# Optimization experiments

Measured on AMD Instinct MI355X. Metric: run time of the kernel, lower is better.

The kernel has to match this reference:

```python
import jax, jax.numpy as jnp
import numpy as np


def setup_inputs() -> dict:
    key = jax.random.key(0)
    k1, k2, k3, k4 = jax.random.split(key, 4)
    b, c, h, w = 16, 1024, 32, 32
    dim = h * w  # 1024
    x = jax.random.normal(k1, (b, c, h, w), dtype=jnp.float32)
    cond_img = jax.random.normal(k2, (b, c, h, w), dtype=jnp.float32)
    # torch nn.Linear weights: (out_features, in_features), y = x @ W.T
    Wq = jax.random.normal(k3, (dim, dim), dtype=jnp.float32) * (dim ** -0.5)
    Wkv = jax.random.normal(k4, (2 * dim, dim), dtype=jnp.float32) * (dim ** -0.5)
    return {"x": x, "cond_img": cond_img, "Wq": Wq, "Wkv": Wkv}


def reference(x, cond_img, Wq, Wkv):
    b, c, h, w = x.shape
    dim = h * w
    scale = dim ** -0.5
    xf = x.reshape(b, c, dim)          # (b, c, dim)
    cf = cond_img.reshape(b, c, dim)   # (b, c, dim)
    q = jnp.einsum('bcd,od->bco', xf, Wq)          # (b, c, dim)
    kv = jnp.einsum('bcd,od->bco', cf, Wkv)        # (b, c, 2*dim)
    k, v = jnp.split(kv, 2, axis=-1)               # each (b, c, dim)
    attn = jnp.einsum('bic,bjc->bij', q, k) * scale  # (b, c, c)
    attn = jax.nn.softmax(attn, axis=-1)
    out = jnp.einsum('bij,bjc->bic', attn, v)      # (b, c, dim)
    return out.reshape(b, c, h, w)
```

## Files before the change

### kernel.cpp

```cpp
#include <hip/hip_runtime.h>
#include <stdint.h>


typedef __bf16 bf16_t;
typedef bf16_t bf16x8 __attribute__((ext_vector_type(8)));
typedef float f32x4 __attribute__((ext_vector_type(4)));

#define AS1 __attribute__((address_space(1)))
#define AS3 __attribute__((address_space(3)))

__device__ __forceinline__ uint16_t f2bf(float f) {
  bf16_t h = (bf16_t)f;
  return __builtin_bit_cast(uint16_t, h);
}

__global__ __launch_bounds__(256) void cvt_all(
    const float* __restrict__ x, const float* __restrict__ c,
    const float* __restrict__ wq, const float* __restrict__ wkv,
    uint16_t* __restrict__ XB, uint16_t* __restrict__ CB,
    uint16_t* __restrict__ WQB, uint16_t* __restrict__ WKVB) {
  long i = (long)blockIdx.x * 256 + threadIdx.x;
  if (i >= 9175040) return;
  const float* src;
  uint16_t* dst;
  long off;
  if (i < 4194304) { src = x; dst = XB; off = i; }
  else if (i < 8388608) { src = c; dst = CB; off = i - 4194304; }
  else if (i < 8650752) { src = wq; dst = WQB; off = i - 8388608; }
  else { src = wkv; dst = WKVB; off = i - 8650752; }
  float4 v = ((const float4*)src)[off];
  ushort4 o;
  o.x = f2bf(v.x); o.y = f2bf(v.y); o.z = f2bf(v.z); o.w = f2bf(v.w);
  ((ushort4*)dst)[off] = o;
}

__device__ __forceinline__ void stage_tile(const uint16_t* __restrict__ g,
                                           int ldK, uint16_t* lds, int tid) {
#pragma unroll
  for (int i = 0; i < 4; ++i) {
    int cix = i * 512 + tid;
    int row = cix >> 3;
    int ch = cix & 7;
    int sch = ch ^ (row & 7);
    const uint16_t* gp = g + row * ldK + sch * 8;
    __builtin_amdgcn_global_load_lds((AS1 void*)gp,
                                     (AS3 void*)((uint8_t*)lds + cix * 16), 16,
                                     0, 0);
  }
}

__device__ __forceinline__ void stage128(const uint16_t* __restrict__ g,
                                         int ldK, uint16_t* lds, int tid) {
#pragma unroll
  for (int i = 0; i < 4; ++i) {
    int cix = i * 256 + tid;
    int row = cix >> 3;
    int ch = cix & 7;
    int sch = ch ^ (row & 7);
    const uint16_t* gp = g + row * ldK + sch * 8;
    __builtin_amdgcn_global_load_lds((AS1 void*)gp,
                                     (AS3 void*)((uint8_t*)lds + cix * 16), 16,
                                     0, 0);
  }
}

__device__ __forceinline__ void xcd_decode(int& bx, int& by, int& bz) {
  const int gx = gridDim.x, gy = gridDim.y;
  const int nwg = gx * gy * gridDim.z;
  int fid = blockIdx.x + gx * (blockIdx.y + gy * blockIdx.z);
  int swz = (fid & 7) * (nwg >> 3) + (fid >> 3);
  bx = swz % gx;
  int rem = swz / gx;
  by = rem % gy;
  bz = rem / gy;
}

__global__ __launch_bounds__(512, 2) void g_kv(
    const uint16_t* __restrict__ A, const uint16_t* __restrict__ B,
    uint16_t* __restrict__ Kp, uint16_t* __restrict__ Vp, int K) {
  __shared__ uint16_t smem[65536];

  const int tid = threadIdx.x;
  const int lane = tid & 63;
  const int wid = tid >> 6;
  const int wr = wid >> 2;
  const int wc = wid & 3;
  const int lr = lane & 15, lg = lane >> 4;
  const int ch0 = lr & 7;

  int bx, by, bz;
  xcd_decode(bx, by, bz);
  const int row0 = by * 256;
  const int col0 = bx * 256;
  const uint16_t* At = A + (long long)row0 * K;
  const uint16_t* Bt = B + (long long)col0 * K;

  const int NT = K >> 6;

  stage_tile(At, K, smem, tid);
  stage_tile(Bt, K, smem + 32768, tid);
  stage_tile(At + 64, K, smem + 16384, tid);
  stage_tile(Bt + 64, K, smem + 49152, tid);
  asm volatile("s_waitcnt vmcnt(8)" ::: "memory");
  __builtin_amdgcn_s_barrier();

  f32x4 acc[8][4] = {};
  bf16x8 aA_[4][2], aB_[4][2], bF[4][2];

  {
    const uint8_t* sa = (const uint8_t*)smem;
#pragma unroll
    for (int mi = 0; mi < 4; ++mi)
#pragma unroll
      for (int kk = 0; kk < 2; ++kk)
        aA_[mi][kk] = *(const bf16x8*)(sa + (wr * 128 + mi * 16 + lr) * 128 +
                                       (((kk * 4 + lg) ^ ch0) << 4));
  }

  for (int t = 0; t < NT; ++t) {
    const uint8_t* sa = (const uint8_t*)(smem + (t & 1) * 16384);
    const uint8_t* sb = (const uint8_t*)(smem + 32768 + (t & 1) * 16384);

#pragma unroll
    for (int nj = 0; nj < 4; ++nj)
#pragma unroll
      for (int kk = 0; kk < 2; ++kk)
        bF[nj][kk] = *(const bf16x8*)(sb + (wc * 64 + nj * 16 + lr) * 128 +
                                      (((kk * 4 + lg) ^ ch0) << 4));
#pragma unroll
    for (int mi = 0; mi < 4; ++mi)
#pragma unroll
      for (int kk = 0; kk < 2; ++kk)
        aB_[mi][kk] = *(const bf16x8*)(sa + (wr * 128 + 64 + mi * 16 + lr) * 128 +
                                       (((kk * 4 + lg) ^ ch0) << 4));
    __builtin_amdgcn_s_setprio(1);
#pragma unroll
    for (int kk = 0; kk < 2; ++kk)
#pragma unroll
      for (int mi = 0; mi < 4; ++mi)
#pragma unroll
        for (int nj = 0; nj < 4; ++nj)
          acc[mi][nj] = __builtin_amdgcn_mfma_f32_16x16x32_bf16(
              aA_[mi][kk], bF[nj][kk], acc[mi][nj], 0, 0, 0);
    __builtin_amdgcn_s_setprio(0);
    if (t + 1 < NT) asm volatile("s_waitcnt vmcnt(4)" ::: "memory");
    asm volatile("s_waitcnt lgkmcnt(0)" ::: "memory");
    __builtin_amdgcn_s_barrier();

    if (t + 2 < NT) {
      stage_tile(At + (t + 2) * 64, K, smem + (t & 1) * 16384, tid);
      stage_tile(Bt + (t + 2) * 64, K, smem + 32768 + (t & 1) * 16384, tid);
    }
    if (t + 1 < NT) {
      const uint8_t* sa2 = (const uint8_t*)(smem + ((t + 1) & 1) * 16384);
#pragma unroll
      for (int mi = 0; mi < 4; ++mi)
#pragma unroll
        for (int kk = 0; kk < 2; ++kk)
          aA_[mi][kk] = *(const bf16x8*)(sa2 + (wr * 128 + mi * 16 + lr) * 128 +
                                         (((kk * 4 + lg) ^ ch0) << 4));
    }
    __builtin_amdgcn_s_setprio(1);
#pragma unroll
    for (int kk = 0; kk < 2; ++kk)
#pragma unroll
      for (int mi = 0; mi < 4; ++mi)
#pragma unroll
        for (int nj = 0; nj < 4; ++nj)
          acc[4 + mi][nj] = __builtin_amdgcn_mfma_f32_16x16x32_bf16(
              aB_[mi][kk], bF[nj][kk], acc[4 + mi][nj], 0, 0, 0);
    __builtin_amdgcn_s_setprio(0);
    if (t + 2 < NT)
      asm volatile("s_waitcnt vmcnt(8)" ::: "memory");
    else
      asm volatile("s_waitcnt vmcnt(0)" ::: "memory");
    __builtin_amdgcn_s_barrier();
  }

  if (col0 >= 1024) {
    __syncthreads();
#pragma unroll
    for (int mi = 0; mi < 8; ++mi) {
#pragma unroll
      for (int ni = 0; ni < 4; ++ni) {
        const int cc = wc * 64 + ni * 16 + lr;
        const int jjb = wr * 128 + mi * 16 + lg * 4;
        ushort4 o;
        o.x = f2bf(acc[mi][ni][0]);
        o.y = f2bf(acc[mi][ni][1]);
        o.z = f2bf(acc[mi][ni][2]);
        o.w = f2bf(acc[mi][ni][3]);
        *(ushort4*)&smem[cc * 256 + (jjb ^ ((cc & 7) << 3))] = o;
      }
    }
    __syncthreads();
    const int b = row0 >> 10, jj0 = row0 & 1023;
#pragma unroll
    for (int k = 0; k < 16; ++k) {
      const int cc = k * 16 + (tid >> 5);
      const int jb = (tid & 31) * 8;
      bf16x8 v = *(const bf16x8*)&smem[cc * 256 + (jb ^ ((cc & 7) << 3))];
      *(bf16x8*)(Vp + (long long)b * 1048576 +
                 (long long)(col0 - 1024 + cc) * 1024 + jj0 + jb) = v;
    }
    return;
  }
#pragma unroll
  for (int mi = 0; mi < 8; ++mi) {
#pragma unroll
    for (int ni = 0; ni < 4; ++ni) {
      const int row = row0 + wr * 128 + mi * 16 + lg * 4;
      const int col = col0 + wc * 64 + ni * 16 + lr;
#pragma unroll
      for (int j = 0; j < 4; ++j)
        Kp[(long long)(row + j) * 1024 + col] = f2bf(acc[mi][ni][j]);
    }
  }
}

template <int EPI>
__device__ __forceinline__ void gemm128_body(
    const uint16_t* __restrict__ A, const uint16_t* __restrict__ B,
    void* __restrict__ C0, float* __restrict__ Rpart, int K, int N,
    long long sA, long long sB, long long sC, float scale) {
  __shared__ uint16_t smem[32768];
  __shared__ float RLDS[128];

  const int tid = threadIdx.x;
  const int lane = tid & 63;
  const int wid = tid >> 6;
  const int wr = wid >> 1;
  const int wc = wid & 1;
  const int lr = lane & 15, lg = lane >> 4;
  const int ch0 = lr & 7;

  int bx, by, bz;
  xcd_decode(bx, by, bz);
  const int row0 = by * 128;
  const int col0 = bx * 128;
  const int grow0 = bz * (N >= 1024 ? 1024 : N) + row0;
  const uint16_t* At = A + (long long)bz * sA + (long long)row0 * K;
  const uint16_t* Bt = B + (long long)bz * sB + (long long)col0 * K;

  const int NT = K >> 6;

  if (EPI == 4) {
    if (tid < 128) {
      float r = 0.f;
#pragma unroll
      for (int p = 0; p < 8; ++p) r += Rpart[p * 16384 + grow0 + tid];
      RLDS[tid] = 1.0f / r;
    }
  }

  stage128(At, K, smem, tid);
  stage128(Bt, K, smem + 16384, tid);
  stage128(At + 64, K, smem + 8192, tid);
  stage128(Bt + 64, K, smem + 24576, tid);
  asm volatile("s_waitcnt vmcnt(8)" ::: "memory");
  __builtin_amdgcn_s_barrier();

  f32x4 acc[4][4] = {};
  bf16x8 aA_[2][2], aB_[2][2], bF[4][2];

  {
    const uint8_t* sa = (const uint8_t*)smem;
#pragma unroll
    for (int mi = 0; mi < 2; ++mi)
#pragma unroll
      for (int kk = 0; kk < 2; ++kk)
        aA_[mi][kk] = *(const bf16x8*)(sa + (wr * 64 + mi * 16 + lr) * 128 +
                                       (((kk * 4 + lg) ^ ch0) << 4));
  }

  for (int t = 0; t < NT; ++t) {
    const uint8_t* sa = (const uint8_t*)(smem + (t & 1) * 8192);
    const uint8_t* sb = (const uint8_t*)(smem + 16384 + (t & 1) * 8192);

#pragma unroll
    for (int nj = 0; nj < 4; ++nj)
#pragma unroll
      for (int kk = 0; kk < 2; ++kk)
        bF[nj][kk] = *(const bf16x8*)(sb + (wc * 64 + nj * 16 + lr) * 128 +
                                      (((kk * 4 + lg) ^ ch0) << 4));
#pragma unroll
    for (int mi = 0; mi < 2; ++mi)
#pragma unroll
      for (int kk = 0; kk < 2; ++kk)
        aB_[mi][kk] = *(const bf16x8*)(sa + (wr * 64 + 32 + mi * 16 + lr) * 128 +
                                       (((kk * 4 + lg) ^ ch0) << 4));
    __builtin_amdgcn_s_setprio(1);
#pragma unroll
    for (int kk = 0; kk < 2; ++kk)
#pragma unroll
      for (int mi = 0; mi < 2; ++mi)
#pragma unroll
        for (int nj = 0; nj < 4; ++nj)
          acc[mi][nj] = __builtin_amdgcn_mfma_f32_16x16x32_bf16(
              aA_[mi][kk], bF[nj][kk], acc[mi][nj], 0, 0, 0);
    __builtin_amdgcn_s_setprio(0);
    if (t + 1 < NT) asm volatile("s_waitcnt vmcnt(4)" ::: "memory");
    asm volatile("s_waitcnt lgkmcnt(0)" ::: "memory");
    __builtin_amdgcn_s_barrier();

    if (t + 2 < NT) {
      stage128(At + (t + 2) * 64, K, smem + (t & 1) * 8192, tid);
      stage128(Bt + (t + 2) * 64, K, smem + 16384 + (t & 1) * 8192, tid);
    }
    if (t + 1 < NT) {
      const uint8_t* sa2 = (const uint8_t*)(smem + ((t + 1) & 1) * 8192);
#pragma unroll
      for (int mi = 0; mi < 2; ++mi)
#pragma unroll
        for (int kk = 0; kk < 2; ++kk)
          aA_[mi][kk] = *(const bf16x8*)(sa2 + (wr * 64 + mi * 16 + lr) * 128 +
                                         (((kk * 4 + lg) ^ ch0) << 4));
    }
    __builtin_amdgcn_s_setprio(1);
#pragma unroll
    for (int kk = 0; kk < 2; ++kk)
#pragma unroll
      for (int mi = 0; mi < 2; ++mi)
#pragma unroll
        for (int nj = 0; nj < 4; ++nj)
          acc[2 + mi][nj] = __builtin_amdgcn_mfma_f32_16x16x32_bf16(
              aB_[mi][kk], bF[nj][kk], acc[2 + mi][nj], 0, 0, 0);
    __builtin_amdgcn_s_setprio(0);
    if (t + 2 < NT)
      asm volatile("s_waitcnt vmcnt(8)" ::: "memory");
    else
      asm volatile("s_waitcnt vmcnt(0)" ::: "memory");
    __builtin_amdgcn_s_barrier();
  }

  if (EPI == 0) {
    uint16_t* C = (uint16_t*)C0;
#pragma unroll
    for (int mi = 0; mi < 4; ++mi)
#pragma unroll
      for (int ni = 0; ni < 4; ++ni) {
        const int row = row0 + wr * 64 + mi * 16 + lg * 4;
        const int col = col0 + wc * 64 + ni * 16 + lr;
#pragma unroll
        for (int j = 0; j < 4; ++j)
          C[(long long)(row + j) * N + col] = f2bf(acc[mi][ni][j]);
      }
  } else if (EPI == 3) {
    uint16_t* Pp = (uint16_t*)C0 + (long long)bz * sC;
    float rs[4][4];
#pragma unroll
    for (int mi = 0; mi < 4; ++mi) {
#pragma unroll
      for (int j = 0; j < 4; ++j) rs[mi][j] = 0.f;
#pragma unroll
      for (int ni = 0; ni < 4; ++ni) {
        const int row = row0 + wr * 64 + mi * 16 + lg * 4;
        const int col = col0 + wc * 64 + ni * 16 + lr;
#pragma unroll
        for (int j = 0; j < 4; ++j) {
          float e = __expf(acc[mi][ni][j] * scale);
          Pp[(long long)(row + j) * N + col] = f2bf(e);
          rs[mi][j] += e;
        }
      }
    }
#pragma unroll
    for (int o = 1; o < 16; o <<= 1)
#pragma unroll
      for (int mi = 0; mi < 4; ++mi)
#pragma unroll
        for (int j = 0; j < 4; ++j) rs[mi][j] += __shfl_xor(rs[mi][j], o, 64);
    __syncthreads();
    float* RS = (float*)smem;
    if (lr == 0) {
#pragma unroll
      for (int mi = 0; mi < 4; ++mi)
#pragma unroll
        for (int j = 0; j < 4; ++j)
          RS[wc * 128 + wr * 64 + mi * 16 + lg * 4 + j] = rs[mi][j];
    }
    __syncthreads();
    if (tid < 128) Rpart[bx * 16384 + grow0 + tid] = RS[tid] + RS[128 + tid];
  } else {
    float* C = (float*)C0;
#pragma unroll
    for (int mi = 0; mi < 4; ++mi)
#pragma unroll
      for (int ni = 0; ni < 4; ++ni) {
        const int row = row0 + wr * 64 + mi * 16 + lg * 4;
        const int col = col0 + wc * 64 + ni * 16 + lr;
#pragma unroll
        for (int j = 0; j < 4; ++j) {
          const float rinv = RLDS[wr * 64 + mi * 16 + lg * 4 + j];
          C[(long long)bz * sC + (long long)(row + j) * N + col] =
              acc[mi][ni][j] * rinv;
        }
      }
  }
}

__global__ __launch_bounds__(256, 2) void g_qproj(const uint16_t* A,
                                                  const uint16_t* B,
                                                  uint16_t* C, int K, int N) {
  gemm128_body<0>(A, B, C, nullptr, K, N, 0, 0, 0, 1.0f);
}
__global__ __launch_bounds__(256, 2) void g_s(const uint16_t* A,
                                              const uint16_t* B, uint16_t* Pp,
                                              float* Rpart, int K,
                                              float scale) {
  gemm128_body<3>(A, B, Pp, Rpart, K, 1024, 1048576, 1048576, 1048576, scale);
}
__global__ __launch_bounds__(256, 2) void g_pv(const uint16_t* A,
                                               const uint16_t* B, float* C,
                                               float* Rpart, int K) {
  gemm128_body<4>(A, B, C, Rpart, K, 1024, 1048576, 1048576, 1048576, 1.0f);
}

extern "C" void kernel_launch(void* const* d_in, const int* in_sizes, int n_in,
                              void* d_out, int out_size, void* d_ws, size_t ws_size,
                              hipStream_t stream) {
  const float* x    = (const float*)d_in[0];
  const float* cond = (const float*)d_in[1];
  const float* Wq   = (const float*)d_in[2];
  const float* Wkv  = (const float*)d_in[3];
  float* out = (float*)d_out;

  uint8_t* ws = (uint8_t*)d_ws;
  const long long MiB = 1ll << 20;
  uint16_t* XB    = (uint16_t*)(ws + 0 * MiB);
  uint16_t* CB    = (uint16_t*)(ws + 32 * MiB);
  uint16_t* Pp    = (uint16_t*)(ws + 0 * MiB);
  float*    Rpart = (float*)(ws + 32 * MiB);
  uint16_t* WQB   = (uint16_t*)(ws + 64 * MiB);
  uint16_t* WKVB  = (uint16_t*)(ws + 66 * MiB);
  uint16_t* Q     = (uint16_t*)(ws + 70 * MiB);
  uint16_t* Kb    = (uint16_t*)(ws + 102 * MiB);
  uint16_t* VT    = (uint16_t*)(ws + 134 * MiB);

  cvt_all<<<35840, 256, 0, stream>>>(x, cond, Wq, Wkv, XB, CB, WQB, WKVB);

  g_qproj<<<dim3(8, 128), 256, 0, stream>>>(XB, WQB, Q, 1024, 1024);
  g_kv<<<dim3(8, 64), 512, 0, stream>>>(CB, WKVB, Kb, VT, 1024);
  g_s<<<dim3(8, 8, 16), 256, 0, stream>>>(Q, Kb, Pp, Rpart, 1024, 0.03125f);
  g_pv<<<dim3(8, 8, 16), 256, 0, stream>>>(Pp, VT, out, Rpart, 1024);
}
```

Before: 236.4 us.

## Fuse x fp32-to-bf16 conversion into Q projection and use 256 tiles for attention GEMMs

```diff
diff --git a/kernel.cpp b/kernel.cpp
--- a/kernel.cpp
+++ b/kernel.cpp
@@ -14,20 +14,18 @@
   return __builtin_bit_cast(uint16_t, h);
 }
 
-__global__ __launch_bounds__(256) void cvt_all(
-    const float* __restrict__ x, const float* __restrict__ c,
-    const float* __restrict__ wq, const float* __restrict__ wkv,
-    uint16_t* __restrict__ XB, uint16_t* __restrict__ CB,
+__global__ __launch_bounds__(256) void cvt2(
+    const float* __restrict__ c, const float* __restrict__ wq,
+    const float* __restrict__ wkv, uint16_t* __restrict__ CB,
     uint16_t* __restrict__ WQB, uint16_t* __restrict__ WKVB) {
   long i = (long)blockIdx.x * 256 + threadIdx.x;
-  if (i >= 9175040) return;
+  if (i >= 4980736) return;
   const float* src;
   uint16_t* dst;
   long off;
-  if (i < 4194304) { src = x; dst = XB; off = i; }
-  else if (i < 8388608) { src = c; dst = CB; off = i - 4194304; }
-  else if (i < 8650752) { src = wq; dst = WQB; off = i - 8388608; }
-  else { src = wkv; dst = WKVB; off = i - 8650752; }
+  if (i < 4194304) { src = c; dst = CB; off = i; }
+  else if (i < 4456448) { src = wq; dst = WQB; off = i - 4194304; }
+  else { src = wkv; dst = WKVB; off = i - 4456448; }
   float4 v = ((const float4*)src)[off];
   ushort4 o;
   o.x = f2bf(v.x); o.y = f2bf(v.y); o.z = f2bf(v.z); o.w = f2bf(v.w);
@@ -75,10 +73,151 @@
   bz = rem / gy;
 }
 
-__global__ __launch_bounds__(512, 2) void g_kv(
+#define ISSUE_AQ(TOFF)                                                        \
+  _Pragma("unroll") for (int kq = 0; kq < 4; ++kq) {                          \
+    int j = kq * 256 + tid;                                                   \
+    const float* gp = At32 + (long long)(j >> 3) * K + (TOFF) + (j & 7) * 8;  \
+    areg[kq][0] = *(const f32x4*)gp;                                          \
+    areg[kq][1] = *(const f32x4*)(gp + 4);                                    \
+  }
+#define WRITE_AQ(BUF)                                                         \
+  _Pragma("unroll") for (int kq = 0; kq < 4; ++kq) {                          \
+    int j = kq * 256 + tid;                                                   \
+    int row = j >> 3, ch = j & 7;                                             \
+    bf16x8 o;                                                                 \
+    o[0] = (bf16_t)areg[kq][0][0]; o[1] = (bf16_t)areg[kq][0][1];             \
+    o[2] = (bf16_t)areg[kq][0][2]; o[3] = (bf16_t)areg[kq][0][3];             \
+    o[4] = (bf16_t)areg[kq][1][0]; o[5] = (bf16_t)areg[kq][1][1];             \
+    o[6] = (bf16_t)areg[kq][1][2]; o[7] = (bf16_t)areg[kq][1][3];             \
+    *(bf16x8*)((uint8_t*)(BUF) + row * 128 + ((ch ^ (row & 7)) << 4)) = o;    \
+  }
+
+__global__ __launch_bounds__(256, 2) void g_qproj(
+    const float* __restrict__ x, const uint16_t* __restrict__ B,
+    uint16_t* __restrict__ C, int K, int N) {
+  __shared__ uint16_t smem[32768];
+
+  const int tid = threadIdx.x;
+  const int lane = tid & 63;
+  const int wid = tid >> 6;
+  const int wr = wid >> 1, wc = wid & 1;
+  const int lr = lane & 15, lg = lane >> 4;
+  const int ch0 = lr & 7;
+
+  int bx, by, bz;
+  xcd_decode(bx, by, bz);
+  const int row0 = by * 128;
+  const int col0 = bx * 128;
+  const float* At32 = x + (long long)row0 * K;
+  const uint16_t* Bt = B + (long long)col0 * K;
+
+  const int NT = K >> 6;
+
+  f32x4 areg[4][2];
+
+  stage128(Bt, K, smem + 16384, tid);
+  stage128(Bt + 64, K, smem + 24576, tid);
+  ISSUE_AQ(0);
+  WRITE_AQ(smem);
+  ISSUE_AQ(64);
+  WRITE_AQ((uint8_t*)smem + 16384);
+  if (NT > 2) ISSUE_AQ(128);
+  asm volatile("s_waitcnt lgkmcnt(0)" ::: "memory");
+  __builtin_amdgcn_s_barrier();
+
+  f32x4 acc[4][4] = {};
+  bf16x8 aA_[2][2], aB_[2][2], bF[4][2];
+
+  {
+    const uint8_t* sa = (const uint8_t*)smem;
+#pragma unroll
+    for (int mi = 0; mi < 2; ++mi)
+#pragma unroll
+      for (int kk = 0; kk < 2; ++kk)
+        aA_[mi][kk] = *(const bf16x8*)(sa + (wr * 64 + mi * 16 + lr) * 128 +
+                                       (((kk * 4 + lg) ^ ch0) << 4));
+  }
+
+  for (int t = 0; t < NT; ++t) {
+    const uint8_t* sa = (const uint8_t*)(smem + (t & 1) * 8192);
+    const uint8_t* sb = (const uint8_t*)(smem + 16384 + (t & 1) * 8192);
+
+#pragma unroll
+    for (int nj = 0; nj < 4; ++nj)
+#pragma unroll
+      for (int kk = 0; kk < 2; ++kk)
+        bF[nj][kk] = *(const bf16x8*)(sb + (wc * 64 + nj * 16 + lr) * 128 +
+                                      (((kk * 4 + lg) ^ ch0) << 4));
+#pragma unroll
+    for (int mi = 0; mi < 2; ++mi)
+#pragma unroll
+      for (int kk = 0; kk < 2; ++kk)
+        aB_[mi][kk] = *(const bf16x8*)(sa + (wr * 64 + 32 + mi * 16 + lr) * 128 +
+                                       (((kk * 4 + lg) ^ ch0) << 4));
+    __builtin_amdgcn_s_setprio(1);
+#pragma unroll
+    for (int kk = 0; kk < 2; ++kk)
+#pragma unroll
+      for (int mi = 0; mi < 2; ++mi)
+#pragma unroll
+        for (int nj = 0; nj < 4; ++nj)
+          acc[mi][nj] = __builtin_amdgcn_mfma_f32_16x16x32_bf16(
+              aA_[mi][kk], bF[nj][kk], acc[mi][nj], 0, 0, 0);
+    __builtin_amdgcn_s_setprio(0);
+    asm volatile("s_waitcnt lgkmcnt(0)" ::: "memory");
+    __builtin_amdgcn_s_barrier();
+
+    if (t + 2 < NT) WRITE_AQ((uint8_t*)smem + (t & 1) * 16384);
+    if (t + 3 < NT) ISSUE_AQ((t + 3) * 64);
+    if (t + 2 < NT)
+      stage128(Bt + (t + 2) * 64, K, smem + 16384 + (t & 1) * 8192, tid);
+    if (t + 1 < NT) {
+      const uint8_t* sa2 = (const uint8_t*)(smem + ((t + 1) & 1) * 8192);
+#pragma unroll
+      for (int mi = 0; mi < 2; ++mi)
+#pragma unroll
+        for (int kk = 0; kk < 2; ++kk)
+          aA_[mi][kk] = *(const bf16x8*)(sa2 + (wr * 64 + mi * 16 + lr) * 128 +
+                                         (((kk * 4 + lg) ^ ch0) << 4));
+    }
+    __builtin_amdgcn_s_setprio(1);
+#pragma unroll
+    for (int kk = 0; kk < 2; ++kk)
+#pragma unroll
+      for (int mi = 0; mi < 2; ++mi)
+#pragma unroll
+        for (int nj = 0; nj < 4; ++nj)
+          acc[2 + mi][nj] = __builtin_amdgcn_mfma_f32_16x16x32_bf16(
+              aB_[mi][kk], bF[nj][kk], acc[2 + mi][nj], 0, 0, 0);
+    __builtin_amdgcn_s_setprio(0);
+    if (t + 3 < NT)
+      asm volatile("s_waitcnt vmcnt(12)" ::: "memory");
+    else if (t + 2 < NT)
+      asm volatile("s_waitcnt vmcnt(4)" ::: "memory");
+    else if (t + 1 < NT)
+      asm volatile("s_waitcnt vmcnt(0)" ::: "memory");
+    __builtin_amdgcn_s_barrier();
+  }
+
+#pragma unroll
+  for (int mi = 0; mi < 4; ++mi)
+#pragma unroll
+    for (int ni = 0; ni < 4; ++ni) {
+      const int row = row0 + wr * 64 + mi * 16 + lg * 4;
+      const int col = col0 + wc * 64 + ni * 16 + lr;
+#pragma unroll
+      for (int j = 0; j < 4; ++j)
+        C[(long long)(row + j) * N + col] = f2bf(acc[mi][ni][j]);
+    }
+}
+
+template <int EPI>
+__device__ __forceinline__ void gemm256_body(
     const uint16_t* __restrict__ A, const uint16_t* __restrict__ B,
-    uint16_t* __restrict__ Kp, uint16_t* __restrict__ Vp, int K) {
+    void* __restrict__ C0, void* __restrict__ C1, float* __restrict__ Rpart,
+    int K, float scale) {
   __shared__ uint16_t smem[65536];
+  __shared__ float RLDS[256];
 
   const int tid = threadIdx.x;
   const int lane = tid & 63;
@@ -92,10 +231,21 @@
   xcd_decode(bx, by, bz);
   const int row0 = by * 256;
   const int col0 = bx * 256;
-  const uint16_t* At = A + (long long)row0 * K;
-  const uint16_t* Bt = B + (long long)col0 * K;
+  const long long sAB = (EPI == 1) ? 0ll : 1048576ll;
+  const uint16_t* At = A + (long long)bz * sAB + (long long)row0 * K;
+  const uint16_t* Bt = B + (long long)bz * sAB + (long long)col0 * K;
+  const int grow0 = bz * 1024 + row0;
 
   const int NT = K >> 6;
+
+  if (EPI == 4) {
+    if (tid < 256) {
+      float r = 0.f;
+#pragma unroll
+      for (int p = 0; p < 4; ++p) r += Rpart[p * 16384 + grow0 + tid];
+      RLDS[tid] = 1.0f / r;
+    }
+  }
 
   stage_tile(At, K, smem, tid);
   stage_tile(Bt, K, smem + 32768, tid);
@@ -177,189 +327,61 @@
     __builtin_amdgcn_s_barrier();
   }
 
-  if (col0 >= 1024) {
-    __syncthreads();
-#pragma unroll
-    for (int mi = 0; mi < 8; ++mi) {
+  if (EPI == 1) {
+    if (col0 >= 1024) {
+      __syncthreads();
+#pragma unroll
+      for (int mi = 0; mi < 8; ++mi)
+#pragma unroll
+        for (int ni = 0; ni < 4; ++ni) {
+          const int cc = wc * 64 + ni * 16 + lr;
+          const int jjb = wr * 128 + mi * 16 + lg * 4;
+          ushort4 o;
+          o.x = f2bf(acc[mi][ni][0]);
+          o.y = f2bf(acc[mi][ni][1]);
+          o.z = f2bf(acc[mi][ni][2]);
+          o.w = f2bf(acc[mi][ni][3]);
+          *(ushort4*)&smem[cc * 256 + (jjb ^ ((cc & 7) << 3))] = o;
+        }
+      __syncthreads();
+      const int b = row0 >> 10, jj0 = row0 & 1023;
+      uint16_t* Vp = (uint16_t*)C1;
+#pragma unroll
+      for (int k = 0; k < 16; ++k) {
+        const int cc = k * 16 + (tid >> 5);
+        const int jb = (tid & 31) * 8;
+        bf16x8 v = *(const bf16x8*)&smem[cc * 256 + (jb ^ ((cc & 7) << 3))];
+        *(bf16x8*)(Vp + (long long)b * 1048576 +
+                   (long long)(col0 - 1024 + cc) * 1024 + jj0 + jb) = v;
+      }
+      return;
+    }
+    uint16_t* Kp = (uint16_t*)C0;
+#pragma unroll
+    for (int mi = 0; mi < 8; ++mi)
 #pragma unroll
       for (int ni = 0; ni < 4; ++ni) {
-        const int cc = wc * 64 + ni * 16 + lr;
-        const int jjb = wr * 128 + mi * 16 + lg * 4;
-        ushort4 o;
-        o.x = f2bf(acc[mi][ni][0]);
-        o.y = f2bf(acc[mi][ni][1]);
-        o.z = f2bf(acc[mi][ni][2]);
-        o.w = f2bf(acc[mi][ni][3]);
-        *(ushort4*)&smem[cc * 256 + (jjb ^ ((cc & 7) << 3))] = o;
-      }
-    }
-    __syncthreads();
-    const int b = row0 >> 10, jj0 = row0 & 1023;
-#pragma unroll
-    for (int k = 0; k < 16; ++k) {
-      const int cc = k * 16 + (tid >> 5);
-      const int jb = (tid & 31) * 8;
-      bf16x8 v = *(const bf16x8*)&smem[cc * 256 + (jb ^ ((cc & 7) << 3))];
-      *(bf16x8*)(Vp + (long long)b * 1048576 +
-                 (long long)(col0 - 1024 + cc) * 1024 + jj0 + jb) = v;
-    }
-    return;
-  }
-#pragma unroll
-  for (int mi = 0; mi < 8; ++mi) {
-#pragma unroll
-    for (int ni = 0; ni < 4; ++ni) {
-      const int row = row0 + wr * 128 + mi * 16 + lg * 4;
-      const int col = col0 + wc * 64 + ni * 16 + lr;
-#pragma unroll
-      for (int j = 0; j < 4; ++j)
-        Kp[(long long)(row + j) * 1024 + col] = f2bf(acc[mi][ni][j]);
-    }
-  }
-}
-
-template <int EPI>
-__device__ __forceinline__ void gemm128_body(
-    const uint16_t* __restrict__ A, const uint16_t* __restrict__ B,
-    void* __restrict__ C0, float* __restrict__ Rpart, int K, int N,
-    long long sA, long long sB, long long sC, float scale) {
-  __shared__ uint16_t smem[32768];
-  __shared__ float RLDS[128];
-
-  const int tid = threadIdx.x;
-  const int lane = tid & 63;
-  const int wid = tid >> 6;
-  const int wr = wid >> 1;
-  const int wc = wid & 1;
-  const int lr = lane & 15, lg = lane >> 4;
-  const int ch0 = lr & 7;
-
-  int bx, by, bz;
-  xcd_decode(bx, by, bz);
-  const int row0 = by * 128;
-  const int col0 = bx * 128;
-  const int grow0 = bz * (N >= 1024 ? 1024 : N) + row0;
-  const uint16_t* At = A + (long long)bz * sA + (long long)row0 * K;
-  const uint16_t* Bt = B + (long long)bz * sB + (long long)col0 * K;
-
-  const int NT = K >> 6;
-
-  if (EPI == 4) {
-    if (tid < 128) {
-      float r = 0.f;
-#pragma unroll
-      for (int p = 0; p < 8; ++p) r += Rpart[p * 16384 + grow0 + tid];
-      RLDS[tid] = 1.0f / r;
-    }
-  }
-
-  stage128(At, K, smem, tid);
-  stage128(Bt, K, smem + 16384, tid);
-  stage128(At + 64, K, smem + 8192, tid);
-  stage128(Bt + 64, K, smem + 24576, tid);
-  asm volatile("s_waitcnt vmcnt(8)" ::: "memory");
-  __builtin_amdgcn_s_barrier();
-
-  f32x4 acc[4][4] = {};
-  bf16x8 aA_[2][2], aB_[2][2], bF[4][2];
-
-  {
-    const uint8_t* sa = (const uint8_t*)smem;
-#pragma unroll
-    for (int mi = 0; mi < 2; ++mi)
-#pragma unroll
-      for (int kk = 0; kk < 2; ++kk)
-        aA_[mi][kk] = *(const bf16x8*)(sa + (wr * 64 + mi * 16 + lr) * 128 +
-                                       (((kk * 4 + lg) ^ ch0) << 4));
-  }
-
-  for (int t = 0; t < NT; ++t) {
-    const uint8_t* sa = (const uint8_t*)(smem + (t & 1) * 8192);
-    const uint8_t* sb = (const uint8_t*)(smem + 16384 + (t & 1) * 8192);
-
-#pragma unroll
-    for (int nj = 0; nj < 4; ++nj)
-#pragma unroll
-      for (int kk = 0; kk < 2; ++kk)
-        bF[nj][kk] = *(const bf16x8*)(sb + (wc * 64 + nj * 16 + lr) * 128 +
-                                      (((kk * 4 + lg) ^ ch0) << 4));
-#pragma unroll
-    for (int mi = 0; mi < 2; ++mi)
-#pragma unroll
-      for (int kk = 0; kk < 2; ++kk)
-        aB_[mi][kk] = *(const bf16x8*)(sa + (wr * 64 + 32 + mi * 16 + lr) * 128 +
-                                       (((kk * 4 + lg) ^ ch0) << 4));
-    __builtin_amdgcn_s_setprio(1);
-#pragma unroll
-    for (int kk = 0; kk < 2; ++kk)
-#pragma unroll
-      for (int mi = 0; mi < 2; ++mi)
-#pragma unroll
-        for (int nj = 0; nj < 4; ++nj)
-          acc[mi][nj] = __builtin_amdgcn_mfma_f32_16x16x32_bf16(
-              aA_[mi][kk], bF[nj][kk], acc[mi][nj], 0, 0, 0);
-    __builtin_amdgcn_s_setprio(0);
-    if (t + 1 < NT) asm volatile("s_waitcnt vmcnt(4)" ::: "memory");
-    asm volatile("s_waitcnt lgkmcnt(0)" ::: "memory");
-    __builtin_amdgcn_s_barrier();
-
-    if (t + 2 < NT) {
-      stage128(At + (t + 2) * 64, K, smem + (t & 1) * 8192, tid);
-      stage128(Bt + (t + 2) * 64, K, smem + 16384 + (t & 1) * 8192, tid);
-    }
-    if (t + 1 < NT) {
-      const uint8_t* sa2 = (const uint8_t*)(smem + ((t + 1) & 1) * 8192);
-#pragma unroll
-      for (int mi = 0; mi < 2; ++mi)
-#pragma unroll
-        for (int kk = 0; kk < 2; ++kk)
-          aA_[mi][kk] = *(const bf16x8*)(sa2 + (wr * 64 + mi * 16 + lr) * 128 +
-                                         (((kk * 4 + lg) ^ ch0) << 4));
-    }
-    __builtin_amdgcn_s_setprio(1);
-#pragma unroll
-    for (int kk = 0; kk < 2; ++kk)
-#pragma unroll
-      for (int mi = 0; mi < 2; ++mi)
-#pragma unroll
-        for (int nj = 0; nj < 4; ++nj)
-          acc[2 + mi][nj] = __builtin_amdgcn_mfma_f32_16x16x32_bf16(
-              aB_[mi][kk], bF[nj][kk], acc[2 + mi][nj], 0, 0, 0);
-    __builtin_amdgcn_s_setprio(0);
-    if (t + 2 < NT)
-      asm volatile("s_waitcnt vmcnt(8)" ::: "memory");
-    else
-      asm volatile("s_waitcnt vmcnt(0)" ::: "memory");
-    __builtin_amdgcn_s_barrier();
-  }
-
-  if (EPI == 0) {
-    uint16_t* C = (uint16_t*)C0;
-#pragma unroll
-    for (int mi = 0; mi < 4; ++mi)
-#pragma unroll
-      for (int ni = 0; ni < 4; ++ni) {
-        const int row = row0 + wr * 64 + mi * 16 + lg * 4;
+        const int row = row0 + wr * 128 + mi * 16 + lg * 4;
         const int col = col0 + wc * 64 + ni * 16 + lr;
 #pragma unroll
         for (int j = 0; j < 4; ++j)
-          C[(long long)(row + j) * N + col] = f2bf(acc[mi][ni][j]);
+          Kp[(long long)(row + j) * 1024 + col] = f2bf(acc[mi][ni][j]);
       }
   } else if (EPI == 3) {
-    uint16_t* Pp = (uint16_t*)C0 + (long long)bz * sC;
-    float rs[4][4];
-#pragma unroll
-    for (int mi = 0; mi < 4; ++mi) {
+    uint16_t* Pp = (uint16_t*)C0 + (long long)bz * 1048576;
+    float rs[8][4];
+#pragma unroll
+    for (int mi = 0; mi < 8; ++mi) {
 #pragma unroll
       for (int j = 0; j < 4; ++j) rs[mi][j] = 0.f;
 #pragma unroll
       for (int ni = 0; ni < 4; ++ni) {
-        const int row = row0 + wr * 64 + mi * 16 + lg * 4;
+        const int row = row0 + wr * 128 + mi * 16 + lg * 4;
         const int col = col0 + wc * 64 + ni * 16 + lr;
 #pragma unroll
         for (int j = 0; j < 4; ++j) {
           float e = __expf(acc[mi][ni][j] * scale);
-          Pp[(long long)(row + j) * N + col] = f2bf(e);
+          Pp[(long long)(row + j) * 1024 + col] = f2bf(e);
           rs[mi][j] += e;
         }
       }
@@ -367,53 +389,55 @@
 #pragma unroll
     for (int o = 1; o < 16; o <<= 1)
 #pragma unroll
-      for (int mi = 0; mi < 4; ++mi)
+      for (int mi = 0; mi < 8; ++mi)
 #pragma unroll
         for (int j = 0; j < 4; ++j) rs[mi][j] += __shfl_xor(rs[mi][j], o, 64);
     __syncthreads();
     float* RS = (float*)smem;
     if (lr == 0) {
 #pragma unroll
-      for (int mi = 0; mi < 4; ++mi)
+      for (int mi = 0; mi < 8; ++mi)
 #pragma unroll
         for (int j = 0; j < 4; ++j)
-          RS[wc * 128 + wr * 64 + mi * 16 + lg * 4 + j] = rs[mi][j];
+          RS[wc * 256 + wr * 128 + mi * 16 + lg * 4 + j] = rs[mi][j];
     }
     __syncthreads();
-    if (tid < 128) Rpart[bx * 16384 + grow0 + tid] = RS[tid] + RS[128 + tid];
+    if (tid < 256)
+      Rpart[bx * 16384 + grow0 + tid] =
+          RS[tid] + RS[256 + tid] + RS[512 + tid] + RS[768 + tid];
   } else {
     float* C = (float*)C0;
 #pragma unroll
-    for (int mi = 0; mi < 4; ++mi)
+    for (int mi = 0; mi < 8; ++mi)
 #pragma unroll
       for (int ni = 0; ni < 4; ++ni) {
-        const int row = row0 + wr * 64 + mi * 16 + lg * 4;
+        const int row = row0 + wr * 128 + mi * 16 + lg * 4;
         const int col = col0 + wc * 64 + ni * 16 + lr;
 #pragma unroll
         for (int j = 0; j < 4; ++j) {
-          const float rinv = RLDS[wr * 64 + mi * 16 + lg * 4 + j];
-          C[(long long)bz * sC + (long long)(row + j) * N + col] =
+          const float rinv = RLDS[wr * 128 + mi * 16 + lg * 4 + j];
+          C[(long long)bz * 1048576 + (long long)(row + j) * 1024 + col] =
               acc[mi][ni][j] * rinv;
         }
       }
   }
 }
 
-__global__ __launch_bounds__(256, 2) void g_qproj(const uint16_t* A,
-                                                  const uint16_t* B,
-                                                  uint16_t* C, int K, int N) {
-  gemm128_body<0>(A, B, C, nullptr, K, N, 0, 0, 0, 1.0f);
-}
-__global__ __launch_bounds__(256, 2) void g_s(const uint16_t* A,
+__global__ __launch_bounds__(512, 2) void g_kv(const uint16_t* A,
+                                               const uint16_t* B, uint16_t* Kp,
+                                               uint16_t* Vp, int K) {
+  gemm256_body<1>(A, B, Kp, Vp, nullptr, K, 1.0f);
+}
+__global__ __launch_bounds__(512, 2) void g_s(const uint16_t* A,
                                               const uint16_t* B, uint16_t* Pp,
                                               float* Rpart, int K,
                                               float scale) {
-  gemm128_body<3>(A, B, Pp, Rpart, K, 1024, 1048576, 1048576, 1048576, scale);
-}
-__global__ __launch_bounds__(256, 2) void g_pv(const uint16_t* A,
+  gemm256_body<3>(A, B, Pp, nullptr, Rpart, K, scale);
+}
+__global__ __launch_bounds__(512, 2) void g_pv(const uint16_t* A,
                                                const uint16_t* B, float* C,
                                                float* Rpart, int K) {
-  gemm128_body<4>(A, B, C, Rpart, K, 1024, 1048576, 1048576, 1048576, 1.0f);
+  gemm256_body<4>(A, B, C, nullptr, Rpart, K, 1.0f);
 }
 
 extern "C" void kernel_launch(void* const* d_in, const int* in_sizes, int n_in,
@@ -427,9 +451,8 @@
 
   uint8_t* ws = (uint8_t*)d_ws;
   const long long MiB = 1ll << 20;
-  uint16_t* XB    = (uint16_t*)(ws + 0 * MiB);
+  uint16_t* Pp    = (uint16_t*)(ws + 0 * MiB);
   uint16_t* CB    = (uint16_t*)(ws + 32 * MiB);
-  uint16_t* Pp    = (uint16_t*)(ws + 0 * MiB);
   float*    Rpart = (float*)(ws + 32 * MiB);
   uint16_t* WQB   = (uint16_t*)(ws + 64 * MiB);
   uint16_t* WKVB  = (uint16_t*)(ws + 66 * MiB);
@@ -437,10 +460,10 @@
   uint16_t* Kb    = (uint16_t*)(ws + 102 * MiB);
   uint16_t* VT    = (uint16_t*)(ws + 134 * MiB);
 
-  cvt_all<<<35840, 256, 0, stream>>>(x, cond, Wq, Wkv, XB, CB, WQB, WKVB);
-
-  g_qproj<<<dim3(8, 128), 256, 0, stream>>>(XB, WQB, Q, 1024, 1024);
+  cvt2<<<19456, 256, 0, stream>>>(cond, Wq, Wkv, CB, WQB, WKVB);
+
+  g_qproj<<<dim3(8, 128), 256, 0, stream>>>(x, WQB, Q, 1024, 1024);
   g_kv<<<dim3(8, 64), 512, 0, stream>>>(CB, WKVB, Kb, VT, 1024);
-  g_s<<<dim3(8, 8, 16), 256, 0, stream>>>(Q, Kb, Pp, Rpart, 1024, 0.03125f);
-  g_pv<<<dim3(8, 8, 16), 256, 0, stream>>>(Pp, VT, out, Rpart, 1024);
-}
+  g_s<<<dim3(4, 4, 16), 512, 0, stream>>>(Q, Kb, Pp, Rpart, 1024, 0.03125f);
+  g_pv<<<dim3(4, 4, 16), 512, 0, stream>>>(Pp, VT, out, Rpart, 1024);
+}
```

Result: slower. 273.3 us (+15.6%).

## Restructure KV GEMM main loop into eight-phase half-tile staged pipeline

Applied to the files above, without the earlier changes.

```diff
diff --git a/kernel.cpp b/kernel.cpp
--- a/kernel.cpp
+++ b/kernel.cpp
@@ -34,17 +34,17 @@
   ((ushort4*)dst)[off] = o;
 }
 
-__device__ __forceinline__ void stage_tile(const uint16_t* __restrict__ g,
+__device__ __forceinline__ void stage_half(const uint16_t* __restrict__ g,
                                            int ldK, uint16_t* lds, int tid) {
 #pragma unroll
-  for (int i = 0; i < 4; ++i) {
-    int cix = i * 512 + tid;
-    int row = cix >> 3;
-    int ch = cix & 7;
+  for (int i = 0; i < 2; ++i) {
+    int c = i * 512 + tid;
+    int row = c >> 3;
+    int ch = c & 7;
     int sch = ch ^ (row & 7);
     const uint16_t* gp = g + row * ldK + sch * 8;
     __builtin_amdgcn_global_load_lds((AS1 void*)gp,
-                                     (AS3 void*)((uint8_t*)lds + cix * 16), 16,
+                                     (AS3 void*)((uint8_t*)lds + c * 16), 16,
                                      0, 0);
   }
 }
@@ -75,10 +75,35 @@
   bz = rem / gy;
 }
 
-__global__ __launch_bounds__(512, 2) void g_kv(
+#define KV_RD_A(BASE, H)                                                      \
+  _Pragma("unroll") for (int mi = 0; mi < 4; ++mi)                            \
+      _Pragma("unroll") for (int kk = 0; kk < 2; ++kk)                        \
+          aF[mi][kk] = *(const bf16x8*)((BASE) + ((H)*64 + mi*16 + lr)*128 +  \
+                                        (((kk*4 + lg) ^ ch0) << 4));
+#define KV_RD_B(BASE, N2)                                                     \
+  _Pragma("unroll") for (int nj = 0; nj < 2; ++nj)                            \
+      _Pragma("unroll") for (int kk = 0; kk < 2; ++kk)                        \
+          bAll[(N2)*2 + nj][kk] = *(const bf16x8*)(                           \
+              (BASE) + ((wc & 1)*64 + ((N2)*2 + nj)*16 + lr)*128 +            \
+              (((kk*4 + lg) ^ ch0) << 4));
+#define KV_MFMA(H, N2)                                                        \
+  __builtin_amdgcn_s_setprio(1);                                              \
+  _Pragma("unroll") for (int kk = 0; kk < 2; ++kk)                            \
+      _Pragma("unroll") for (int mi = 0; mi < 4; ++mi)                        \
+          _Pragma("unroll") for (int nj = 0; nj < 2; ++nj)                    \
+              acc[(H)*4 + mi][(N2)*2 + nj] =                                  \
+                  __builtin_amdgcn_mfma_f32_16x16x32_bf16(                    \
+                      aF[mi][kk], bAll[(N2)*2 + nj][kk],                      \
+                      acc[(H)*4 + mi][(N2)*2 + nj], 0, 0, 0);                 \
+  __builtin_amdgcn_s_setprio(0);
+#define KV_BAR __builtin_amdgcn_s_barrier()
+#define KV_LGKM0 asm volatile("s_waitcnt lgkmcnt(0)" ::: "memory")
+
+__global__ __launch_bounds__(512) void g_kv(
     const uint16_t* __restrict__ A, const uint16_t* __restrict__ B,
     uint16_t* __restrict__ Kp, uint16_t* __restrict__ Vp, int K) {
-  __shared__ uint16_t smem[65536];
+  __shared__ uint16_t As[2][2][8192];
+  __shared__ uint16_t Bs[2][2][8192];
 
   const int tid = threadIdx.x;
   const int lane = tid & 63;
@@ -96,91 +121,87 @@
   const uint16_t* Bt = B + (long long)col0 * K;
 
   const int NT = K >> 6;
-
-  stage_tile(At, K, smem, tid);
-  stage_tile(Bt, K, smem + 32768, tid);
-  stage_tile(At + 64, K, smem + 16384, tid);
-  stage_tile(Bt + 64, K, smem + 49152, tid);
-  asm volatile("s_waitcnt vmcnt(8)" ::: "memory");
-  __builtin_amdgcn_s_barrier();
+  const int NIT = NT >> 1;
+
+  stage_half(Bt, K, &Bs[0][0][0], tid);
+  stage_half(Bt + 128 * K, K, &Bs[0][1][0], tid);
+  stage_half(At, K, &As[0][0][0], tid);
+  stage_half(At + 128 * K, K, &As[0][1][0], tid);
+  stage_half(Bt + 64, K, &Bs[1][0][0], tid);
+  stage_half(Bt + 128 * K + 64, K, &Bs[1][1][0], tid);
+  asm volatile("s_waitcnt vmcnt(4)" ::: "memory");
+  KV_BAR;
 
   f32x4 acc[8][4] = {};
-  bf16x8 aA_[4][2], aB_[4][2], bF[4][2];
-
-  {
-    const uint8_t* sa = (const uint8_t*)smem;
-#pragma unroll
-    for (int mi = 0; mi < 4; ++mi)
-#pragma unroll
-      for (int kk = 0; kk < 2; ++kk)
-        aA_[mi][kk] = *(const bf16x8*)(sa + (wr * 128 + mi * 16 + lr) * 128 +
-                                       (((kk * 4 + lg) ^ ch0) << 4));
-  }
-
-  for (int t = 0; t < NT; ++t) {
-    const uint8_t* sa = (const uint8_t*)(smem + (t & 1) * 16384);
-    const uint8_t* sb = (const uint8_t*)(smem + 32768 + (t & 1) * 16384);
-
-#pragma unroll
-    for (int nj = 0; nj < 4; ++nj)
-#pragma unroll
-      for (int kk = 0; kk < 2; ++kk)
-        bF[nj][kk] = *(const bf16x8*)(sb + (wc * 64 + nj * 16 + lr) * 128 +
-                                      (((kk * 4 + lg) ^ ch0) << 4));
-#pragma unroll
-    for (int mi = 0; mi < 4; ++mi)
-#pragma unroll
-      for (int kk = 0; kk < 2; ++kk)
-        aB_[mi][kk] = *(const bf16x8*)(sa + (wr * 128 + 64 + mi * 16 + lr) * 128 +
-                                       (((kk * 4 + lg) ^ ch0) << 4));
-    __builtin_amdgcn_s_setprio(1);
-#pragma unroll
-    for (int kk = 0; kk < 2; ++kk)
-#pragma unroll
-      for (int mi = 0; mi < 4; ++mi)
-#pragma unroll
-        for (int nj = 0; nj < 4; ++nj)
-          acc[mi][nj] = __builtin_amdgcn_mfma_f32_16x16x32_bf16(
-              aA_[mi][kk], bF[nj][kk], acc[mi][nj], 0, 0, 0);
-    __builtin_amdgcn_s_setprio(0);
-    if (t + 1 < NT) asm volatile("s_waitcnt vmcnt(4)" ::: "memory");
-    asm volatile("s_waitcnt lgkmcnt(0)" ::: "memory");
-    __builtin_amdgcn_s_barrier();
-
-    if (t + 2 < NT) {
-      stage_tile(At + (t + 2) * 64, K, smem + (t & 1) * 16384, tid);
-      stage_tile(Bt + (t + 2) * 64, K, smem + 32768 + (t & 1) * 16384, tid);
-    }
-    if (t + 1 < NT) {
-      const uint8_t* sa2 = (const uint8_t*)(smem + ((t + 1) & 1) * 16384);
-#pragma unroll
-      for (int mi = 0; mi < 4; ++mi)
-#pragma unroll
-        for (int kk = 0; kk < 2; ++kk)
-          aA_[mi][kk] = *(const bf16x8*)(sa2 + (wr * 128 + mi * 16 + lr) * 128 +
-                                         (((kk * 4 + lg) ^ ch0) << 4));
-    }
-    __builtin_amdgcn_s_setprio(1);
-#pragma unroll
-    for (int kk = 0; kk < 2; ++kk)
-#pragma unroll
-      for (int mi = 0; mi < 4; ++mi)
-#pragma unroll
-        for (int nj = 0; nj < 4; ++nj)
-          acc[4 + mi][nj] = __builtin_amdgcn_mfma_f32_16x16x32_bf16(
-              aB_[mi][kk], bF[nj][kk], acc[4 + mi][nj], 0, 0, 0);
-    __builtin_amdgcn_s_setprio(0);
-    if (t + 2 < NT)
-      asm volatile("s_waitcnt vmcnt(8)" ::: "memory");
+  bf16x8 aF[4][2];
+  bf16x8 bAll[4][2];
+
+  for (int i = 0; i < NIT; ++i) {
+    const int t1 = 2 * i + 1, tn0 = 2 * i + 2, tn1 = 2 * i + 3;
+    const uint8_t* a0 = (const uint8_t*)&As[0][wr][0];
+    const uint8_t* a1 = (const uint8_t*)&As[1][wr][0];
+    const uint8_t* b0 = (const uint8_t*)&Bs[0][wc >> 1][0];
+    const uint8_t* b1 = (const uint8_t*)&Bs[1][wc >> 1][0];
+
+    KV_RD_A(a0, 0);
+    KV_RD_B(b0, 0);
+    stage_half(At + t1 * 64, K, &As[1][0][0], tid);
+    KV_BAR; KV_LGKM0;
+    KV_MFMA(0, 0);
+    KV_BAR;
+
+    KV_RD_B(b0, 1);
+    stage_half(At + 128 * K + t1 * 64, K, &As[1][1][0], tid);
+    KV_BAR; KV_LGKM0;
+    KV_MFMA(0, 1);
+    KV_BAR;
+
+    KV_RD_A(a0, 1);
+    if (tn0 < NT) stage_half(Bt + tn0 * 64, K, &Bs[0][0][0], tid);
+    KV_BAR; KV_LGKM0;
+    KV_MFMA(1, 0);
+    KV_BAR;
+
+    if (tn0 < NT) stage_half(Bt + 128 * K + tn0 * 64, K, &Bs[0][1][0], tid);
+    KV_BAR; KV_LGKM0;
+    KV_MFMA(1, 1);
+    if (i + 1 < NIT)
+      asm volatile("s_waitcnt vmcnt(4)" ::: "memory");
     else
       asm volatile("s_waitcnt vmcnt(0)" ::: "memory");
-    __builtin_amdgcn_s_barrier();
+    KV_BAR;
+
+    KV_RD_A(a1, 0);
+    KV_RD_B(b1, 0);
+    if (tn0 < NT) stage_half(At + tn0 * 64, K, &As[0][0][0], tid);
+    KV_BAR; KV_LGKM0;
+    KV_MFMA(0, 0);
+    KV_BAR;
+
+    KV_RD_B(b1, 1);
+    if (tn0 < NT) stage_half(At + 128 * K + tn0 * 64, K, &As[0][1][0], tid);
+    KV_BAR; KV_LGKM0;
+    KV_MFMA(0, 1);
+    KV_BAR;
+
+    KV_RD_A(a1, 1);
+    if (tn1 < NT) stage_half(Bt + tn1 * 64, K, &Bs[1][0][0], tid);
+    KV_BAR; KV_LGKM0;
+    KV_MFMA(1, 0);
+    KV_BAR;
+
+    if (tn1 < NT) stage_half(Bt + 128 * K + tn1 * 64, K, &Bs[1][1][0], tid);
+    KV_BAR; KV_LGKM0;
+    KV_MFMA(1, 1);
+    if (i + 1 < NIT) asm volatile("s_waitcnt vmcnt(4)" ::: "memory");
+    KV_BAR;
   }
 
   if (col0 >= 1024) {
     __syncthreads();
-#pragma unroll
-    for (int mi = 0; mi < 8; ++mi) {
+    uint16_t* smem = &As[0][0][0];
+#pragma unroll
+    for (int mi = 0; mi < 8; ++mi)
 #pragma unroll
       for (int ni = 0; ni < 4; ++ni) {
         const int cc = wc * 64 + ni * 16 + lr;
@@ -192,7 +213,6 @@
         o.w = f2bf(acc[mi][ni][3]);
         *(ushort4*)&smem[cc * 256 + (jjb ^ ((cc & 7) << 3))] = o;
       }
-    }
     __syncthreads();
     const int b = row0 >> 10, jj0 = row0 & 1023;
 #pragma unroll
@@ -206,7 +226,7 @@
     return;
   }
 #pragma unroll
-  for (int mi = 0; mi < 8; ++mi) {
+  for (int mi = 0; mi < 8; ++mi)
 #pragma unroll
     for (int ni = 0; ni < 4; ++ni) {
       const int row = row0 + wr * 128 + mi * 16 + lg * 4;
@@ -215,7 +235,6 @@
       for (int j = 0; j < 4; ++j)
         Kp[(long long)(row + j) * 1024 + col] = f2bf(acc[mi][ni][j]);
     }
-  }
 }
 
 template <int EPI>
@@ -229,8 +248,7 @@
   const int tid = threadIdx.x;
   const int lane = tid & 63;
   const int wid = tid >> 6;
-  const int wr = wid >> 1;
-  const int wc = wid & 1;
+  const int wr = wid >> 1, wc = wid & 1;
   const int lr = lane & 15, lg = lane >> 4;
   const int ch0 = lr & 7;
 
```

Result: slower. 241.6 us (+2.2%).
